# Optimization experiments

Measured on AMD Instinct MI355X. Metric: run time of the kernel, lower is better.

The kernel has to match this reference:

```python
import jax, jax.numpy as jnp
import numpy as np

K = 20
EPS = 1e-5


def knn_idx(x, k):
    # x: (B, N, C) -> (B, N, k) indices of k nearest neighbors (incl. self)
    xx = jnp.sum(x * x, axis=-1, keepdims=True)           # (B,N,1)
    inner = -2.0 * jnp.einsum('bnc,bmc->bnm', x, x)        # (B,N,N)
    pd = -xx - inner - jnp.swapaxes(xx, 1, 2)              # negative sq dist
    _, idx = jax.lax.top_k(pd, k)                          # (B,N,k)
    return idx


def get_graph_feature(x, k=K):
    B, N, C = x.shape
    idx = knn_idx(x, k)                                    # (B,N,k)
    # gather neighbor features per batch
    feature = jax.vmap(lambda xb, ib: xb[ib])(x, idx)      # (B,N,k,C)
    xe = jnp.broadcast_to(x[:, :, None, :], (B, N, k, C))  # (B,N,k,C)
    f = jnp.concatenate([feature - xe, xe], axis=3)        # (B,N,k,2C)
    return jnp.transpose(f, (0, 3, 1, 2))                  # (B,2C,N,k)


def conv1x1(x, W, b):
    # x: (B,Cin,N,k), W: (Cout,Cin)
    return jnp.einsum('bcnk,oc->bonk', x, W) + b[None, :, None, None]


def batchnorm(x, gamma, beta):
    # training-mode BN over (B,N,k) per channel, biased variance (torch default)
    mean = jnp.mean(x, axis=(0, 2, 3), keepdims=True)
    var = jnp.var(x, axis=(0, 2, 3), keepdims=True)
    xhat = (x - mean) * jax.lax.rsqrt(var + EPS)
    return xhat * gamma[None, :, None, None] + beta[None, :, None, None]


def setup_inputs() -> dict:
    key = jax.random.key(0)
    ks = jax.random.split(key, 10)
    B, N, C = 4, 4096, 3
    x = jax.random.normal(ks[0], (B, N, C), dtype=jnp.float32)
    W1 = jax.random.normal(ks[1], (64, 2 * C), dtype=jnp.float32) * 0.1
    b1 = jnp.zeros((64,), jnp.float32)
    g1 = jnp.ones((64,), jnp.float32)
    be1 = jnp.zeros((64,), jnp.float32)
    W2 = jax.random.normal(ks[2], (128, 64), dtype=jnp.float32) * 0.1
    b2 = jnp.zeros((128,), jnp.float32)
    g2 = jnp.ones((128,), jnp.float32)
    be2 = jnp.zeros((128,), jnp.float32)
    W3 = jax.random.normal(ks[3], (128, 128), dtype=jnp.float32) * 0.1
    b3 = jnp.zeros((128,), jnp.float32)
    g3 = jnp.ones((128,), jnp.float32)
    be3 = jnp.zeros((128,), jnp.float32)
    return {"x": x, "W1": W1, "b1": b1, "g1": g1, "be1": be1,
            "W2": W2, "b2": b2, "g2": g2, "be2": be2,
            "W3": W3, "b3": b3, "g3": g3, "be3": be3}


def reference(x, W1, b1, g1, be1, W2, b2, g2, be2, W3, b3, g3, be3):
    f = get_graph_feature(x, K)                  # (B,6,N,k)
    h = jax.nn.relu(batchnorm(conv1x1(f, W1, b1), g1, be1))
    h = jax.nn.relu(batchnorm(conv1x1(h, W2, b2), g2, be2))
    h = batchnorm(conv1x1(h, W3, b3), g3, be3)
    return jnp.max(h, axis=-1)                   # (B,128,N)
```

## Files before the change

### kernel.cpp

```cpp
#include <hip/hip_runtime.h>


typedef __attribute__((ext_vector_type(8)))  short short8;
typedef __attribute__((ext_vector_type(4)))  float floatx4;

#define BATCH 4
#define NPTS  4096
#define KNN   20
#define BN_   (BATCH*NPTS)
#define CNT   (BATCH*NPTS*KNN)

__device__ __forceinline__ unsigned short f2bf(float f) {
  unsigned u = __float_as_uint(f);
  unsigned r = u + 0x7FFFu + ((u >> 16) & 1u);
  return (unsigned short)(r >> 16);
}

__device__ __forceinline__ unsigned cvtpk(float lo, float hi) {
  unsigned r;
  asm("v_cvt_pk_bf16_f32 %0, %1, %2" : "=v"(r) : "v"(lo), "v"(hi));
  return r;
}

union PK8 { unsigned u4[4]; short8 s; };

__device__ __forceinline__ void store4bf_relu(unsigned short* dst, floatx4 v) {
  unsigned lo = cvtpk(fmaxf(v[0],0.f), fmaxf(v[1],0.f));
  unsigned hi = cvtpk(fmaxf(v[2],0.f), fmaxf(v[3],0.f));
  *(uint2*)dst = make_uint2(lo, hi);
}

__device__ __forceinline__ unsigned mono(float f) {
  unsigned u = __float_as_uint(f);
  return u ^ ((unsigned)((int)u >> 31) | 0x80000000u);
}

__device__ __forceinline__ void bn_affine(float gsum, float gsq, float gamma,
                                          float beta, float& s, float& sh) {
  const float inv = 1.0f / (float)CNT;
  float mean = gsum * inv;
  float var  = gsq * inv - mean * mean;
  s  = gamma * rsqrtf(var + 1e-5f);
  sh = beta - mean * s;
}

__global__ void pf_prep(const float* __restrict__ x, float4* __restrict__ xp,
                        float* __restrict__ stats,
                        const float* __restrict__ W2, const float* __restrict__ W3,
                        unsigned short* __restrict__ w2p,
                        unsigned short* __restrict__ w3p) {
  int pt = blockIdx.x * 256 + threadIdx.x;
  float x0 = x[pt*3+0], x1 = x[pt*3+1], x2 = x[pt*3+2];
  float xx = x0*x0 + x1*x1 + x2*x2;
  xp[pt] = make_float4(x0, x1, x2, xx);
  if (blockIdx.x == 0)
    for (int i = threadIdx.x; i < 640; i += 256) stats[i] = 0.0f;
  if (blockIdx.x == 1) {
    for (int i = threadIdx.x; i < 128*64;  i += 256) w2p[i] = f2bf(W2[i]);
    for (int i = threadIdx.x; i < 128*128; i += 256) w3p[i] = f2bf(W3[i]);
  }
}

__device__ __forceinline__ float sort_take20th(float v, int lane) {
  #pragma unroll
  for (int k = 2; k <= 64; k <<= 1) {
    #pragma unroll
    for (int j = k >> 1; j >= 1; j >>= 1) {
      float o = __shfl_xor(v, j);
      bool keepmax = (((lane & j) == 0) == ((lane & k) == 0));
      v = keepmax ? fmaxf(v, o) : fminf(v, o);
    }
  }
  return __shfl(v, 19);
}

__device__ __forceinline__ unsigned long long sort64_desc(unsigned long long v,
                                                          int lane) {
  #pragma unroll
  for (int k = 2; k <= 64; k <<= 1) {
    #pragma unroll
    for (int j = k >> 1; j >= 1; j >>= 1) {
      unsigned long long o = __shfl_xor(v, j);
      bool keepmax = (((lane & j) == 0) == ((lane & k) == 0));
      unsigned long long hi = v > o ? v : o;
      unsigned long long lo = v > o ? o : v;
      v = keepmax ? hi : lo;
    }
  }
  return v;
}

__global__ __launch_bounds__(256) void pf_knn(const float4* __restrict__ xp,
                                              int* __restrict__ idxb) {
  __shared__ unsigned long long lst[16][128];
  __shared__ int lcnt[16];
  const int tid  = threadIdx.x;
  const int lane = tid & 63;
  const int w    = tid >> 6;
  const int b    = blockIdx.x >> 8;
  const int nb   = (blockIdx.x & 255) * 16 + w * 4;
  const float4* xb = xp + b * NPTS;

  float4 q0 = xb[nb], q1 = xb[nb+1], q2 = xb[nb+2], q3 = xb[nb+3];

  float mx0=-3.0e38f, mx1=-3.0e38f, mx2=-3.0e38f, mx3=-3.0e38f;
  for (int j0 = 0; j0 < NPTS; j0 += 64) {
    float4 c = xb[j0 + lane];
    float d0 = fmaf(q0.x,c.x, fmaf(q0.y,c.y, q0.z*c.z));
    float d1 = fmaf(q1.x,c.x, fmaf(q1.y,c.y, q1.z*c.z));
    float d2 = fmaf(q2.x,c.x, fmaf(q2.y,c.y, q2.z*c.z));
    float d3 = fmaf(q3.x,c.x, fmaf(q3.y,c.y, q3.z*c.z));
    mx0 = fmaxf(mx0, fmaf(2.f,d0,-q0.w) - c.w);
    mx1 = fmaxf(mx1, fmaf(2.f,d1,-q1.w) - c.w);
    mx2 = fmaxf(mx2, fmaf(2.f,d2,-q2.w) - c.w);
    mx3 = fmaxf(mx3, fmaf(2.f,d3,-q3.w) - c.w);
  }
  float T0 = sort_take20th(mx0, lane);
  float T1 = sort_take20th(mx1, lane);
  float T2 = sort_take20th(mx2, lane);
  float T3 = sort_take20th(mx3, lane);

  if (lane < 4) lcnt[w*4 + lane] = 0;
  __syncthreads();

  for (int j0 = 0; j0 < NPTS; j0 += 64) {
    float4 c = xb[j0 + lane];
    float d0 = fmaf(q0.x,c.x, fmaf(q0.y,c.y, q0.z*c.z));
    float d1 = fmaf(q1.x,c.x, fmaf(q1.y,c.y, q1.z*c.z));
    float d2 = fmaf(q2.x,c.x, fmaf(q2.y,c.y, q2.z*c.z));
    float d3 = fmaf(q3.x,c.x, fmaf(q3.y,c.y, q3.z*c.z));
    float p0 = fmaf(2.f,d0,-q0.w) - c.w;
    float p1 = fmaf(2.f,d1,-q1.w) - c.w;
    float p2 = fmaf(2.f,d2,-q2.w) - c.w;
    float p3 = fmaf(2.f,d3,-q3.w) - c.w;
    unsigned long long keybase = (unsigned long long)(4095 - (j0 + lane));
    if (p0 >= T0) {
      int o = atomicAdd(&lcnt[w*4+0], 1);
      if (o < 128) lst[w*4+0][o] = ((unsigned long long)mono(p0) << 32) | keybase;
    }
    if (p1 >= T1) {
      int o = atomicAdd(&lcnt[w*4+1], 1);
      if (o < 128) lst[w*4+1][o] = ((unsigned long long)mono(p1) << 32) | keybase;
    }
    if (p2 >= T2) {
      int o = atomicAdd(&lcnt[w*4+2], 1);
      if (o < 128) lst[w*4+2][o] = ((unsigned long long)mono(p2) << 32) | keybase;
    }
    if (p3 >= T3) {
      int o = atomicAdd(&lcnt[w*4+3], 1);
      if (o < 128) lst[w*4+3][o] = ((unsigned long long)mono(p3) << 32) | keybase;
    }
  }

  #pragma unroll 1
  for (int i = 0; i < 4; ++i) {
    const int li = w*4 + i;
    const int cn = lcnt[li];
    const int outbase = (b * NPTS + nb + i) * KNN;
    if (cn <= 64) {
      unsigned long long v = (lane < cn) ? lst[li][lane] : 0ull;
      v = sort64_desc(v, lane);
      if (lane < KNN) idxb[outbase + lane] = 4095 - (int)(v & 0xFFFFFFFFull);
    } else if (cn <= 128) {
      unsigned long long e0 = lst[li][lane];
      unsigned long long e1 = (lane + 64 < cn) ? lst[li][lane + 64] : 0ull;
      #pragma unroll 1
      for (int r = 0; r < KNN; ++r) {
        unsigned long long m = e0 > e1 ? e0 : e1;
        #pragma unroll
        for (int o = 32; o; o >>= 1) {
          unsigned long long t = __shfl_xor(m, o);
          m = t > m ? t : m;
        }
        if (lane == 0) idxb[outbase + r] = 4095 - (int)(m & 0xFFFFFFFFull);
        if (e0 == m) e0 = 0ull; else if (e1 == m) e1 = 0ull;
      }
    } else {
      const float4 qq = (i == 0) ? q0 : (i == 1) ? q1 : (i == 2) ? q2 : q3;
      unsigned long long prev = ~0ull;
      #pragma unroll 1
      for (int r = 0; r < KNN; ++r) {
        unsigned long long best = 0ull;
        for (int j0 = 0; j0 < NPTS; j0 += 64) {
          float4 c = xb[j0 + lane];
          float dd = fmaf(qq.x,c.x, fmaf(qq.y,c.y, qq.z*c.z));
          float pd = fmaf(2.f,dd,-qq.w) - c.w;
          unsigned long long key = ((unsigned long long)mono(pd) << 32) |
                                   (unsigned long long)(4095 - (j0 + lane));
          if (key < prev && key > best) best = key;
        }
        #pragma unroll
        for (int o = 32; o; o >>= 1) {
          unsigned long long t = __shfl_xor(best, o);
          best = t > best ? t : best;
        }
        if (lane == 0) idxb[outbase + r] = 4095 - (int)(best & 0xFFFFFFFFull);
        prev = best;
      }
    }
  }
}

__global__ __launch_bounds__(256) void pf_mom(
    const float4* __restrict__ xp, const int* __restrict__ idxb,
    float* __restrict__ gm) {
  __shared__ float WM[4][27];
  const int tid = threadIdx.x, lane = tid & 63, w = tid >> 6;
  const int pt = blockIdx.x * 256 + tid;
  const float4 xi = xp[pt];
  const int ib = (pt >> 12) << 12;

  int idx[KNN];
  const int4* ip = (const int4*)(idxb + pt*KNN);
  #pragma unroll
  for (int q = 0; q < 5; ++q) {
    int4 v = ip[q];
    idx[q*4+0]=v.x; idx[q*4+1]=v.y; idx[q*4+2]=v.z; idx[q*4+3]=v.w;
  }
  float sj0=0,sj1=0,sj2=0, p0=0,p1=0,p2=0,p3=0,p4=0,p5=0;
  #pragma unroll
  for (int kk = 0; kk < KNN; ++kk) {
    float4 xj = xp[ib + idx[kk]];
    sj0 += xj.x; sj1 += xj.y; sj2 += xj.z;
    p0 = fmaf(xj.x,xj.x,p0); p1 = fmaf(xj.x,xj.y,p1); p2 = fmaf(xj.x,xj.z,p2);
    p3 = fmaf(xj.y,xj.y,p3); p4 = fmaf(xj.y,xj.z,p4); p5 = fmaf(xj.z,xj.z,p5);
  }
  float m[27];
  m[0]=sj0; m[1]=sj1; m[2]=sj2;
  m[3]=20.f*xi.x; m[4]=20.f*xi.y; m[5]=20.f*xi.z;
  m[6]=p0; m[7]=p1; m[8]=p2; m[9]=p3; m[10]=p4; m[11]=p5;
  m[12]=20.f*xi.x*xi.x; m[13]=20.f*xi.x*xi.y; m[14]=20.f*xi.x*xi.z;
  m[15]=20.f*xi.y*xi.y; m[16]=20.f*xi.y*xi.z; m[17]=20.f*xi.z*xi.z;
  m[18]=sj0*xi.x; m[19]=sj0*xi.y; m[20]=sj0*xi.z;
  m[21]=sj1*xi.x; m[22]=sj1*xi.y; m[23]=sj1*xi.z;
  m[24]=sj2*xi.x; m[25]=sj2*xi.y; m[26]=sj2*xi.z;
  #pragma unroll
  for (int c = 0; c < 27; ++c) {
    float v = m[c];
    #pragma unroll
    for (int o = 32; o; o >>= 1) v += __shfl_xor(v, o);
    m[c] = v;
  }
  if (lane == 0)
    #pragma unroll
    for (int c = 0; c < 27; ++c) WM[w][c] = m[c];
  __syncthreads();
  if (tid < 27) atomicAdd(&gm[tid], WM[0][tid]+WM[1][tid]+WM[2][tid]+WM[3][tid]);
}

__global__ void pf_affine1(const float* __restrict__ gm,
                           const float* __restrict__ W1,
                           const float* __restrict__ g1,
                           const float* __restrict__ be1,
                           unsigned short* __restrict__ w1s,
                           float* __restrict__ sh1e) {
  int c = threadIdx.x;
  if (c >= 64) return;
  const float* wr = W1 + c*6;
  const float wa[3] = {wr[0], wr[1], wr[2]};
  const float wb[3] = {wr[3], wr[4], wr[5]};
  const int si0[9] = {0,1,2, 1,3,4, 2,4,5};
  float syf = 0.f, sy2 = 0.f;
  #pragma unroll
  for (int a = 0; a < 3; ++a)
    syf += wa[a]*(gm[a] - gm[3+a]) + wb[a]*gm[3+a];
  #pragma unroll
  for (int a = 0; a < 3; ++a)
    #pragma unroll
    for (int bq = 0; bq < 3; ++bq) {
      int k = a*3 + bq, kt = bq*3 + a;
      float pjj = gm[6 + si0[k]], pii = gm[12 + si0[k]];
      float cc = gm[18 + k], ct = gm[18 + kt];
      float uu = pjj - cc - ct + pii;
      float uv = cc - pii;
      sy2 += wa[a]*wa[bq]*uu + 2.f*wa[a]*wb[bq]*uv + wb[a]*wb[bq]*pii;
    }
  const float inv = 1.0f / (float)CNT;
  float mean = syf * inv;
  float var  = sy2 * inv - mean * mean;
  float s  = g1[c] * rsqrtf(var + 1e-5f);
  sh1e[c]  = be1[c] - mean * s;
  unsigned short* o = w1s + c*8;
  o[0]=f2bf(s*wa[0]); o[1]=f2bf(s*wa[1]); o[2]=f2bf(s*wa[2]);
  o[3]=f2bf(s*wb[0]); o[4]=f2bf(s*wb[1]); o[5]=f2bf(s*wb[2]);
  o[6]=0; o[7]=0;
}

__global__ void pf_affine2(const float* __restrict__ gs2,
                           const float* __restrict__ gq2,
                           const float* __restrict__ W2,
                           const float* __restrict__ g2,
                           const float* __restrict__ be2,
                           unsigned short* __restrict__ w2s,
                           float* __restrict__ shm2) {
  int c = threadIdx.x;
  if (c >= 128) return;
  float s, sh; bn_affine(gs2[c], gq2[c], g2[c], be2[c], s, sh);
  shm2[c] = sh;
  const float* wr = W2 + c*64;
  unsigned short* o = w2s + c*64;
  for (int j = 0; j < 64; ++j) o[j] = f2bf(s * wr[j]);
}

__global__ __launch_bounds__(256, 4) void pf_stats2(
    const float4* __restrict__ xp, const int* __restrict__ idxb,
    const unsigned short* __restrict__ w1s, const float* __restrict__ sh1e,
    const unsigned short* __restrict__ w2p,
    float* __restrict__ gs2, float* __restrict__ gq2) {
  __shared__ __align__(16) short8 AF[KNN][16];
  __shared__ __align__(16) unsigned short H1[2][16][72];
  __shared__ float SS[128], SQ[128];

  const int tid = threadIdx.x;
  const int lane = tid & 63, ww = tid >> 6;
  const int l15 = lane & 15, quad = lane >> 4;
  const int pt0 = blockIdx.x * 16;

  if (tid < 128) { SS[tid] = 0.f; SQ[tid] = 0.f; }

  for (int u = tid; u < 16*KNN; u += 256) {
    int kk = u >> 4, pp = u & 15;
    int pt = pt0 + pp;
    float4 xi = xp[pt];
    float4 xj = xp[((pt >> 12) << 12) + idxb[pt*KNN + kk]];
    PK8 U;
    U.u4[0] = cvtpk(xj.x-xi.x, xj.y-xi.y);
    U.u4[1] = cvtpk(xj.z-xi.z, xi.x);
    U.u4[2] = cvtpk(xi.y, xi.z);
    U.u4[3] = 0;
    AF[kk][pp] = U.s;
  }

  short8 w1f = *(const short8*)(w1s + (16*ww + l15)*8);
  floatx4 sh1v;
  #pragma unroll
  for (int r = 0; r < 4; ++r) sh1v[r] = sh1e[16*ww + 4*quad + r];

  short8 w2f[2][2];
  #pragma unroll
  for (int ks = 0; ks < 2; ++ks)
    #pragma unroll
    for (int t = 0; t < 2; ++t)
      w2f[ks][t] = *(const short8*)(w2p + (32*ww + 16*t + l15)*64 + 32*ks + quad*8);

  float sum[2][4] = {{0,0,0,0},{0,0,0,0}}, sq[2][4] = {{0,0,0,0},{0,0,0,0}};
  const short8 z8 = {0,0,0,0,0,0,0,0};
  __syncthreads();

  #pragma unroll 1
  for (int k = 0; k < KNN + 1; ++k) {
    if (k >= 1) {
      floatx4 acc2[2] = {{0,0,0,0},{0,0,0,0}};
      #pragma unroll
      for (int ks = 0; ks < 2; ++ks) {
        short8 a = *(const short8*)&H1[(k-1) & 1][l15][ks*32 + quad*8];
        #pragma unroll
        for (int t = 0; t < 2; ++t)
          acc2[t] = __builtin_amdgcn_mfma_f32_16x16x32_bf16(w2f[ks][t], a, acc2[t], 0,0,0);
      }
      #pragma unroll
      for (int t = 0; t < 2; ++t)
        #pragma unroll
        for (int r = 0; r < 4; ++r) {
          float v = acc2[t][r];
          sum[t][r] += v; sq[t][r] = fmaf(v, v, sq[t][r]);
        }
    }
    if (k < KNN) {
      short8 a0 = z8;
      if (quad == 0) a0 = AF[k][l15];
      floatx4 c0 = sh1v;
      c0 = __builtin_amdgcn_mfma_f32_16x16x32_bf16(w1f, a0, c0, 0,0,0);
      store4bf_relu(&H1[k & 1][l15][16*ww + 4*quad], c0);
    }
    __syncthreads();
  }
  #pragma unroll
  for (int t = 0; t < 2; ++t)
    #pragma unroll
    for (int r = 0; r < 4; ++r) {
      float s = sum[t][r], z = sq[t][r];
      s += __shfl_xor(s, 1); z += __shfl_xor(z, 1);
      s += __shfl_xor(s, 2); z += __shfl_xor(z, 2);
      s += __shfl_xor(s, 4); z += __shfl_xor(z, 4);
      s += __shfl_xor(s, 8); z += __shfl_xor(z, 8);
      if (l15 == 0) {
        int ch = 32*ww + 16*t + 4*quad + r;
        atomicAdd(&SS[ch], s); atomicAdd(&SQ[ch], z);
      }
    }
  __syncthreads();
  if (tid < 128) { atomicAdd(&gs2[tid], SS[tid]); atomicAdd(&gq2[tid], SQ[tid]); }
}

__global__ __launch_bounds__(256, 4) void pf_main(
    const float4* __restrict__ xp, const int* __restrict__ idxb,
    const unsigned short* __restrict__ w1s, const float* __restrict__ sh1e,
    const unsigned short* __restrict__ w2s, const float* __restrict__ shm2,
    const unsigned short* __restrict__ w3p,
    float* __restrict__ gs3, float* __restrict__ gq3,
    float* __restrict__ maxv) {
  __shared__ __align__(16) short8 AF[KNN][16];
  __shared__ __align__(16) unsigned short H1[2][16][72];
  __shared__ __align__(16) unsigned short H2[2][16][136];
  __shared__ float SS[128], SQ[128];

  const int tid = threadIdx.x;
  const int lane = tid & 63, ww = tid >> 6;
  const int l15 = lane & 15, quad = lane >> 4;
  const int pt0 = blockIdx.x * 16;

  if (tid < 128) { SS[tid] = 0.f; SQ[tid] = 0.f; }

  for (int u = tid; u < 16*KNN; u += 256) {
    int kk = u >> 4, pp = u & 15;
    int pt = pt0 + pp;
    float4 xi = xp[pt];
    float4 xj = xp[((pt >> 12) << 12) + idxb[pt*KNN + kk]];
    PK8 U;
    U.u4[0] = cvtpk(xj.x-xi.x, xj.y-xi.y);
    U.u4[1] = cvtpk(xj.z-xi.z, xi.x);
    U.u4[2] = cvtpk(xi.y, xi.z);
    U.u4[3] = 0;
    AF[kk][pp] = U.s;
  }

  short8 w1f = *(const short8*)(w1s + (16*ww + l15)*8);
  floatx4 sh1v;
  #pragma unroll
  for (int r = 0; r < 4; ++r) sh1v[r] = sh1e[16*ww + 4*quad + r];
  short8 w2f[2][2];
  #pragma unroll
  for (int ks = 0; ks < 2; ++ks)
    #pragma unroll
    for (int t = 0; t < 2; ++t)
      w2f[ks][t] = *(const short8*)(w2s + (32*ww + 16*t + l15)*64 + 32*ks + quad*8);
  floatx4 sh2v[2];
  #pragma unroll
  for (int t = 0; t < 2; ++t)
    #pragma unroll
    for (int r = 0; r < 4; ++r)
      sh2v[t][r] = shm2[32*ww + 16*t + 4*quad + r];
  short8 w3f[4][2];
  #pragma unroll
  for (int ks = 0; ks < 4; ++ks)
    #pragma unroll
    for (int t = 0; t < 2; ++t)
      w3f[ks][t] = *(const short8*)(w3p + (32*ww + 16*t + l15)*128 + 32*ks + quad*8);

  float sum[2][4] = {{0,0,0,0},{0,0,0,0}}, sq[2][4] = {{0,0,0,0},{0,0,0,0}};
  float mx[2][4];
  #pragma unroll
  for (int t = 0; t < 2; ++t)
    #pragma unroll
    for (int r = 0; r < 4; ++r) mx[t][r] = -3.0e38f;

  const short8 z8 = {0,0,0,0,0,0,0,0};
  __syncthreads();

  #pragma unroll 1
  for (int k = 0; k < KNN + 2; ++k) {
    if (k >= 2) {
      floatx4 acc3[2] = {{0,0,0,0},{0,0,0,0}};
      #pragma unroll
      for (int ks = 0; ks < 4; ++ks) {
        short8 a = *(const short8*)&H2[k & 1][l15][ks*32 + quad*8];
        #pragma unroll
        for (int t = 0; t < 2; ++t)
          acc3[t] = __builtin_amdgcn_mfma_f32_16x16x32_bf16(w3f[ks][t], a, acc3[t], 0,0,0);
      }
      #pragma unroll
      for (int t = 0; t < 2; ++t)
        #pragma unroll
        for (int r = 0; r < 4; ++r) {
          float v = acc3[t][r];
          sum[t][r] += v; sq[t][r] = fmaf(v, v, sq[t][r]);
          mx[t][r] = fmaxf(mx[t][r], v);
        }
    }
    if (k >= 1 && k < KNN + 1) {
      floatx4 acc2[2] = {sh2v[0], sh2v[1]};
      #pragma unroll
      for (int ks = 0; ks < 2; ++ks) {
        short8 a = *(const short8*)&H1[(k-1) & 1][l15][ks*32 + quad*8];
        #pragma unroll
        for (int t = 0; t < 2; ++t)
          acc2[t] = __builtin_amdgcn_mfma_f32_16x16x32_bf16(w2f[ks][t], a, acc2[t], 0,0,0);
      }
      #pragma unroll
      for (int t = 0; t < 2; ++t)
        store4bf_relu(&H2[(k-1) & 1][l15][32*ww + 16*t + 4*quad], acc2[t]);
    }
    if (k < KNN) {
      short8 a0 = z8;
      if (quad == 0) a0 = AF[k][l15];
      floatx4 acc1 = sh1v;
      acc1 = __builtin_amdgcn_mfma_f32_16x16x32_bf16(w1f, a0, acc1, 0,0,0);
      store4bf_relu(&H1[k & 1][l15][16*ww + 4*quad], acc1);
    }
    __syncthreads();
  }

  #pragma unroll
  for (int t = 0; t < 2; ++t) {
    int ch0 = 32*ww + 16*t + 4*quad;
    float4 o = make_float4(mx[t][0], mx[t][1], mx[t][2], mx[t][3]);
    *(float4*)&maxv[(size_t)(pt0 + l15)*128 + ch0] = o;
  }
  #pragma unroll
  for (int t = 0; t < 2; ++t)
    #pragma unroll
    for (int r = 0; r < 4; ++r) {
      float s = sum[t][r], z = sq[t][r];
      s += __shfl_xor(s, 1); z += __shfl_xor(z, 1);
      s += __shfl_xor(s, 2); z += __shfl_xor(z, 2);
      s += __shfl_xor(s, 4); z += __shfl_xor(z, 4);
      s += __shfl_xor(s, 8); z += __shfl_xor(z, 8);
      if (l15 == 0) {
        int ch = 32*ww + 16*t + 4*quad + r;
        atomicAdd(&SS[ch], s); atomicAdd(&SQ[ch], z);
      }
    }
  __syncthreads();
  if (tid < 128) { atomicAdd(&gs3[tid], SS[tid]); atomicAdd(&gq3[tid], SQ[tid]); }
}

__global__ __launch_bounds__(256) void pf_out(
    const float* __restrict__ maxv,
    const float* __restrict__ gs3, const float* __restrict__ gq3,
    const float* __restrict__ g3, const float* __restrict__ be3,
    float* __restrict__ out) {
  __shared__ float T[128][17];
  __shared__ float SC[128], SH[128];
  const int tid = threadIdx.x;
  const int b  = blockIdx.x >> 8;
  const int n0 = (blockIdx.x & 255) * 16;
  if (tid < 128) {
    float s, sh; bn_affine(gs3[tid], gq3[tid], g3[tid], be3[tid], s, sh);
    SC[tid] = s; SH[tid] = sh;
  }
  __syncthreads();
  const float4* mv4 = (const float4*)maxv;
  #pragma unroll
  for (int r = 0; r < 2; ++r) {
    int fid = r * 256 + tid;
    int nl = fid >> 5, c4 = fid & 31;
    float4 v = mv4[(size_t)(b*NPTS + n0 + nl)*32 + c4];
    int c = c4 * 4;
    T[c+0][nl] = fmaf(SC[c+0], v.x, SH[c+0]);
    T[c+1][nl] = fmaf(SC[c+1], v.y, SH[c+1]);
    T[c+2][nl] = fmaf(SC[c+2], v.z, SH[c+2]);
    T[c+3][nl] = fmaf(SC[c+3], v.w, SH[c+3]);
  }
  __syncthreads();
  #pragma unroll
  for (int r = 0; r < 2; ++r) {
    int fid = r * 256 + tid;
    int c = fid >> 2, nq = fid & 3;
    float4 o;
    o.x = T[c][nq*4+0]; o.y = T[c][nq*4+1];
    o.z = T[c][nq*4+2]; o.w = T[c][nq*4+3];
    *(float4*)(out + (size_t)b*128*NPTS + (size_t)c*NPTS + n0 + nq*4) = o;
  }
}

extern "C" void kernel_launch(void* const* d_in, const int* in_sizes, int n_in,
                              void* d_out, int out_size, void* d_ws, size_t ws_size,
                              hipStream_t stream) {
  const float* x   = (const float*)d_in[0];
  const float* W1  = (const float*)d_in[1];
  const float* g1  = (const float*)d_in[3];
  const float* be1 = (const float*)d_in[4];
  const float* W2  = (const float*)d_in[5];
  const float* g2  = (const float*)d_in[7];
  const float* be2 = (const float*)d_in[8];
  const float* W3  = (const float*)d_in[9];
  const float* g3  = (const float*)d_in[11];
  const float* be3 = (const float*)d_in[12];
  float* out = (float*)d_out;

  char* p = (char*)d_ws;
  float4* xp  = (float4*)p;            p += (size_t)BN_ * 16;
  int*    idxb= (int*)p;               p += (size_t)BN_ * KNN * 4;
  float*  stats = (float*)p;           p += 640 * 4;
  float*  aff   = (float*)p;           p += 256 * 4;
  unsigned short* w1s = (unsigned short*)p; p += 64 * 8 * 2;
  unsigned short* w2p = (unsigned short*)p; p += 128 * 64 * 2;
  unsigned short* w2s = (unsigned short*)p; p += 128 * 64 * 2;
  unsigned short* w3p = (unsigned short*)p; p += 128 * 128 * 2;
  float*  maxv  = (float*)p;

  float *gm  = stats;
  float *gs2 = stats + 128, *gq2 = stats + 256;
  float *gs3 = stats + 384, *gq3 = stats + 512;
  float *sh1e = aff, *shm2 = aff + 64;

  pf_prep   <<<64,   256, 0, stream>>>(x, xp, stats, W2, W3, w2p, w3p);
  pf_knn    <<<1024, 256, 0, stream>>>(xp, idxb);
  pf_mom    <<<64,   256, 0, stream>>>(xp, idxb, gm);
  pf_affine1<<<1,    64,  0, stream>>>(gm, W1, g1, be1, w1s, sh1e);
  pf_stats2 <<<1024, 256, 0, stream>>>(xp, idxb, w1s, sh1e, w2p, gs2, gq2);
  pf_affine2<<<1,    128, 0, stream>>>(gs2, gq2, W2, g2, be2, w2s, shm2);
  pf_main   <<<1024, 256, 0, stream>>>(xp, idxb, w1s, sh1e, w2s, shm2,
                                       w3p, gs3, gq3, maxv);
  pf_out    <<<1024, 256, 0, stream>>>(maxv, gs3, gq3, g3, be3, out);
}
```

Before: 228.8 us.

## Process 32 points per block in stats2 and main kernels

Doubles the points handled per block in pf_stats2 and pf_main from 16 to 32, running two 16-point MFMA phases per neighbor step and halving the grid. Weight fragments held in registers are reused across twice as many points, and the per-step __syncthreads and block-level atomic reductions are amortized over more work. The cost is more registers and LDS per block (launch bounds lowered to 3 and 2), and only 512 blocks, which may underfill the GPU's compute units.

After: 206.7 us. -9.6%, faster.

```diff
diff --git a/kernel.cpp b/kernel.cpp
--- a/kernel.cpp
+++ b/kernel.cpp
@@ -302,24 +302,24 @@
   for (int j = 0; j < 64; ++j) o[j] = f2bf(s * wr[j]);
 }
 
-__global__ __launch_bounds__(256, 4) void pf_stats2(
+__global__ __launch_bounds__(256, 3) void pf_stats2(
     const float4* __restrict__ xp, const int* __restrict__ idxb,
     const unsigned short* __restrict__ w1s, const float* __restrict__ sh1e,
     const unsigned short* __restrict__ w2p,
     float* __restrict__ gs2, float* __restrict__ gq2) {
-  __shared__ __align__(16) short8 AF[KNN][16];
-  __shared__ __align__(16) unsigned short H1[2][16][72];
+  __shared__ __align__(16) short8 AF[KNN][32];
+  __shared__ __align__(16) unsigned short H1[2][32][72];
   __shared__ float SS[128], SQ[128];
 
   const int tid = threadIdx.x;
   const int lane = tid & 63, ww = tid >> 6;
   const int l15 = lane & 15, quad = lane >> 4;
-  const int pt0 = blockIdx.x * 16;
+  const int pt0 = blockIdx.x * 32;
 
   if (tid < 128) { SS[tid] = 0.f; SQ[tid] = 0.f; }
 
-  for (int u = tid; u < 16*KNN; u += 256) {
-    int kk = u >> 4, pp = u & 15;
+  for (int u = tid; u < 32*KNN; u += 256) {
+    int kk = u >> 5, pp = u & 31;
     int pt = pt0 + pp;
     float4 xi = xp[pt];
     float4 xj = xp[((pt >> 12) << 12) + idxb[pt*KNN + kk]];
@@ -343,35 +343,42 @@
     for (int t = 0; t < 2; ++t)
       w2f[ks][t] = *(const short8*)(w2p + (32*ww + 16*t + l15)*64 + 32*ks + quad*8);
 
-  float sum[2][4] = {{0,0,0,0},{0,0,0,0}}, sq[2][4] = {{0,0,0,0},{0,0,0,0}};
+  float sum[2][2][4] = {{{0,0,0,0},{0,0,0,0}},{{0,0,0,0},{0,0,0,0}}};
+  float sq [2][2][4] = {{{0,0,0,0},{0,0,0,0}},{{0,0,0,0},{0,0,0,0}}};
   const short8 z8 = {0,0,0,0,0,0,0,0};
   __syncthreads();
 
   #pragma unroll 1
   for (int k = 0; k < KNN + 1; ++k) {
     if (k >= 1) {
-      floatx4 acc2[2] = {{0,0,0,0},{0,0,0,0}};
       #pragma unroll
-      for (int ks = 0; ks < 2; ++ks) {
-        short8 a = *(const short8*)&H1[(k-1) & 1][l15][ks*32 + quad*8];
+      for (int ph = 0; ph < 2; ++ph) {
+        floatx4 acc2[2] = {{0,0,0,0},{0,0,0,0}};
+        #pragma unroll
+        for (int ks = 0; ks < 2; ++ks) {
+          short8 a = *(const short8*)&H1[(k-1) & 1][ph*16 + l15][ks*32 + quad*8];
+          #pragma unroll
+          for (int t = 0; t < 2; ++t)
+            acc2[t] = __builtin_amdgcn_mfma_f32_16x16x32_bf16(w2f[ks][t], a, acc2[t], 0,0,0);
+        }
         #pragma unroll
         for (int t = 0; t < 2; ++t)
-          acc2[t] = __builtin_amdgcn_mfma_f32_16x16x32_bf16(w2f[ks][t], a, acc2[t], 0,0,0);
-      }
+          #pragma unroll
+          for (int r = 0; r < 4; ++r) {
+            float v = acc2[t][r];
+            sum[ph][t][r] += v; sq[ph][t][r] = fmaf(v, v, sq[ph][t][r]);
+          }
+      }
+    }
+    if (k < KNN) {
       #pragma unroll
-      for (int t = 0; t < 2; ++t)
-        #pragma unroll
-        for (int r = 0; r < 4; ++r) {
-          float v = acc2[t][r];
-          sum[t][r] += v; sq[t][r] = fmaf(v, v, sq[t][r]);
-        }
-    }
-    if (k < KNN) {
-      short8 a0 = z8;
-      if (quad == 0) a0 = AF[k][l15];
-      floatx4 c0 = sh1v;
-      c0 = __builtin_amdgcn_mfma_f32_16x16x32_bf16(w1f, a0, c0, 0,0,0);
-      store4bf_relu(&H1[k & 1][l15][16*ww + 4*quad], c0);
+      for (int ph = 0; ph < 2; ++ph) {
+        short8 a0 = z8;
+        if (quad == 0) a0 = AF[k][ph*16 + l15];
+        floatx4 c0 = sh1v;
+        c0 = __builtin_amdgcn_mfma_f32_16x16x32_bf16(w1f, a0, c0, 0,0,0);
+        store4bf_relu(&H1[k & 1][ph*16 + l15][16*ww + 4*quad], c0);
+      }
     }
     __syncthreads();
   }
@@ -379,7 +386,8 @@
   for (int t = 0; t < 2; ++t)
     #pragma unroll
     for (int r = 0; r < 4; ++r) {
-      float s = sum[t][r], z = sq[t][r];
+      float s = sum[0][t][r] + sum[1][t][r];
+      float z = sq[0][t][r] + sq[1][t][r];
       s += __shfl_xor(s, 1); z += __shfl_xor(z, 1);
       s += __shfl_xor(s, 2); z += __shfl_xor(z, 2);
       s += __shfl_xor(s, 4); z += __shfl_xor(z, 4);
@@ -393,27 +401,27 @@
   if (tid < 128) { atomicAdd(&gs2[tid], SS[tid]); atomicAdd(&gq2[tid], SQ[tid]); }
 }
 
-__global__ __launch_bounds__(256, 4) void pf_main(
+__global__ __launch_bounds__(256, 2) void pf_main(
     const float4* __restrict__ xp, const int* __restrict__ idxb,
     const unsigned short* __restrict__ w1s, const float* __restrict__ sh1e,
     const unsigned short* __restrict__ w2s, const float* __restrict__ shm2,
     const unsigned short* __restrict__ w3p,
     float* __restrict__ gs3, float* __restrict__ gq3,
     float* __restrict__ maxv) {
-  __shared__ __align__(16) short8 AF[KNN][16];
-  __shared__ __align__(16) unsigned short H1[2][16][72];
-  __shared__ __align__(16) unsigned short H2[2][16][136];
+  __shared__ __align__(16) short8 AF[KNN][32];
+  __shared__ __align__(16) unsigned short H1[2][32][72];
+  __shared__ __align__(16) unsigned short H2[2][32][136];
   __shared__ float SS[128], SQ[128];
 
   const int tid = threadIdx.x;
   const int lane = tid & 63, ww = tid >> 6;
   const int l15 = lane & 15, quad = lane >> 4;
-  const int pt0 = blockIdx.x * 16;
+  const int pt0 = blockIdx.x * 32;
 
   if (tid < 128) { SS[tid] = 0.f; SQ[tid] = 0.f; }
 
-  for (int u = tid; u < 16*KNN; u += 256) {
-    int kk = u >> 4, pp = u & 15;
+  for (int u = tid; u < 32*KNN; u += 256) {
+    int kk = u >> 5, pp = u & 31;
     int pt = pt0 + pp;
     float4 xi = xp[pt];
     float4 xj = xp[((pt >> 12) << 12) + idxb[pt*KNN + kk]];
@@ -448,12 +456,15 @@
     for (int t = 0; t < 2; ++t)
       w3f[ks][t] = *(const short8*)(w3p + (32*ww + 16*t + l15)*128 + 32*ks + quad*8);
 
-  float sum[2][4] = {{0,0,0,0},{0,0,0,0}}, sq[2][4] = {{0,0,0,0},{0,0,0,0}};
-  float mx[2][4];
-  #pragma unroll
-  for (int t = 0; t < 2; ++t)
-    #pragma unroll
-    for (int r = 0; r < 4; ++r) mx[t][r] = -3.0e38f;
+  float sum[2][2][4] = {{{0,0,0,0},{0,0,0,0}},{{0,0,0,0},{0,0,0,0}}};
+  float sq [2][2][4] = {{{0,0,0,0},{0,0,0,0}},{{0,0,0,0},{0,0,0,0}}};
+  float mx [2][2][4];
+  #pragma unroll
+  for (int ph = 0; ph < 2; ++ph)
+    #pragma unroll
+    for (int t = 0; t < 2; ++t)
+      #pragma unroll
+      for (int r = 0; r < 4; ++r) mx[ph][t][r] = -3.0e38f;
 
   const short8 z8 = {0,0,0,0,0,0,0,0};
   __syncthreads();
@@ -461,57 +472,69 @@
   #pragma unroll 1
   for (int k = 0; k < KNN + 2; ++k) {
     if (k >= 2) {
-      floatx4 acc3[2] = {{0,0,0,0},{0,0,0,0}};
       #pragma unroll
-      for (int ks = 0; ks < 4; ++ks) {
-        short8 a = *(const short8*)&H2[k & 1][l15][ks*32 + quad*8];
+      for (int ph = 0; ph < 2; ++ph) {
+        floatx4 acc3[2] = {{0,0,0,0},{0,0,0,0}};
+        #pragma unroll
+        for (int ks = 0; ks < 4; ++ks) {
+          short8 a = *(const short8*)&H2[k & 1][ph*16 + l15][ks*32 + quad*8];
+          #pragma unroll
+          for (int t = 0; t < 2; ++t)
+            acc3[t] = __builtin_amdgcn_mfma_f32_16x16x32_bf16(w3f[ks][t], a, acc3[t], 0,0,0);
+        }
         #pragma unroll
         for (int t = 0; t < 2; ++t)
-          acc3[t] = __builtin_amdgcn_mfma_f32_16x16x32_bf16(w3f[ks][t], a, acc3[t], 0,0,0);
-      }
+          #pragma unroll
+          for (int r = 0; r < 4; ++r) {
+            float v = acc3[t][r];
+            sum[ph][t][r] += v; sq[ph][t][r] = fmaf(v, v, sq[ph][t][r]);
+            mx[ph][t][r] = fmaxf(mx[ph][t][r], v);
+          }
+      }
+    }
+    if (k >= 1 && k < KNN + 1) {
       #pragma unroll
-      for (int t = 0; t < 2; ++t)
-        #pragma unroll
-        for (int r = 0; r < 4; ++r) {
-          float v = acc3[t][r];
-          sum[t][r] += v; sq[t][r] = fmaf(v, v, sq[t][r]);
-          mx[t][r] = fmaxf(mx[t][r], v);
+      for (int ph = 0; ph < 2; ++ph) {
+        floatx4 acc2[2] = {sh2v[0], sh2v[1]};
+        #pragma unroll
+        for (int ks = 0; ks < 2; ++ks) {
+          short8 a = *(const short8*)&H1[(k-1) & 1][ph*16 + l15][ks*32 + quad*8];
+          #pragma unroll
+          for (int t = 0; t < 2; ++t)
+            acc2[t] = __builtin_amdgcn_mfma_f32_16x16x32_bf16(w2f[ks][t], a, acc2[t], 0,0,0);
         }
-    }
-    if (k >= 1 && k < KNN + 1) {
-      floatx4 acc2[2] = {sh2v[0], sh2v[1]};
+        #pragma unroll
+        for (int t = 0; t < 2; ++t)
+          store4bf_relu(&H2[(k-1) & 1][ph*16 + l15][32*ww + 16*t + 4*quad], acc2[t]);
+      }
+    }
+    if (k < KNN) {
       #pragma unroll
-      for (int ks = 0; ks < 2; ++ks) {
-        short8 a = *(const short8*)&H1[(k-1) & 1][l15][ks*32 + quad*8];
-        #pragma unroll
-        for (int t = 0; t < 2; ++t)
-          acc2[t] = __builtin_amdgcn_mfma_f32_16x16x32_bf16(w2f[ks][t], a, acc2[t], 0,0,0);
-      }
-      #pragma unroll
-      for (int t = 0; t < 2; ++t)
-        store4bf_relu(&H2[(k-1) & 1][l15][32*ww + 16*t + 4*quad], acc2[t]);
-    }
-    if (k < KNN) {
-      short8 a0 = z8;
-      if (quad == 0) a0 = AF[k][l15];
-      floatx4 acc1 = sh1v;
-      acc1 = __builtin_amdgcn_mfma_f32_16x16x32_bf16(w1f, a0, acc1, 0,0,0);
-      store4bf_relu(&H1[k & 1][l15][16*ww + 4*quad], acc1);
+      for (int ph = 0; ph < 2; ++ph) {
+        short8 a0 = z8;
+        if (quad == 0) a0 = AF[k][ph*16 + l15];
+        floatx4 acc1 = sh1v;
+        acc1 = __builtin_amdgcn_mfma_f32_16x16x32_bf16(w1f, a0, acc1, 0,0,0);
+        store4bf_relu(&H1[k & 1][ph*16 + l15][16*ww + 4*quad], acc1);
+      }
     }
     __syncthreads();
   }
 
   #pragma unroll
-  for (int t = 0; t < 2; ++t) {
-    int ch0 = 32*ww + 16*t + 4*quad;
-    float4 o = make_float4(mx[t][0], mx[t][1], mx[t][2], mx[t][3]);
-    *(float4*)&maxv[(size_t)(pt0 + l15)*128 + ch0] = o;
-  }
+  for (int ph = 0; ph < 2; ++ph)
+    #pragma unroll
+    for (int t = 0; t < 2; ++t) {
+      int ch0 = 32*ww + 16*t + 4*quad;
+      float4 o = make_float4(mx[ph][t][0], mx[ph][t][1], mx[ph][t][2], mx[ph][t][3]);
+      *(float4*)&maxv[(size_t)(pt0 + ph*16 + l15)*128 + ch0] = o;
+    }
   #pragma unroll
   for (int t = 0; t < 2; ++t)
     #pragma unroll
     for (int r = 0; r < 4; ++r) {
-      float s = sum[t][r], z = sq[t][r];
+      float s = sum[0][t][r] + sum[1][t][r];
+      float z = sq[0][t][r] + sq[1][t][r];
       s += __shfl_xor(s, 1); z += __shfl_xor(z, 1);
       s += __shfl_xor(s, 2); z += __shfl_xor(z, 2);
       s += __shfl_xor(s, 4); z += __shfl_xor(z, 4);
@@ -599,9 +622,9 @@
   pf_knn    <<<1024, 256, 0, stream>>>(xp, idxb);
   pf_mom    <<<64,   256, 0, stream>>>(xp, idxb, gm);
   pf_affine1<<<1,    64,  0, stream>>>(gm, W1, g1, be1, w1s, sh1e);
-  pf_stats2 <<<1024, 256, 0, stream>>>(xp, idxb, w1s, sh1e, w2p, gs2, gq2);
+  pf_stats2 <<<512,  256, 0, stream>>>(xp, idxb, w1s, sh1e, w2p, gs2, gq2);
   pf_affine2<<<1,    128, 0, stream>>>(gs2, gq2, W2, g2, be2, w2s, shm2);
-  pf_main   <<<1024, 256, 0, stream>>>(xp, idxb, w1s, sh1e, w2s, shm2,
+  pf_main   <<<512,  256, 0, stream>>>(xp, idxb, w1s, sh1e, w2s, shm2,
                                        w3p, gs3, gq3, maxv);
   pf_out    <<<1024, 256, 0, stream>>>(maxv, gs3, gq3, g3, be3, out);
 }
```
